# Performance work log

Hardware: AMD Instinct MI355X
Metric: run time of the kernel (lower is better)

## Reference

```python
import jax, jax.numpy as jnp
import numpy as np

EPS = 1e-10


def setup_inputs() -> dict:
    key = jax.random.key(0)
    ks = jax.random.split(key, 8)
    N, C, H, W = 32, 512, 14, 14
    D, HID = 2048, 256
    s1 = 1.0 / np.sqrt(C + D)
    s2 = 1.0 / np.sqrt(HID)
    return {
        "local_feature": jax.random.normal(ks[0], (N, C, H, W), jnp.float32),
        "global_feature": jax.random.normal(ks[1], (N, D, 1, 1), jnp.float32),
        "W1": jax.random.normal(ks[2], (C + D, HID), jnp.float32) * s1,
        "b1": jnp.zeros((HID,), jnp.float32),
        "W2": jax.random.normal(ks[3], (HID, HID), jnp.float32) * s2,
        "b2": jnp.zeros((HID,), jnp.float32),
        "W3": jax.random.normal(ks[4], (HID, 1), jnp.float32) * s2,
        "b3": jnp.zeros((1,), jnp.float32),
    }


def reference(local_feature, global_feature, W1, b1, W2, b2, W3, b3):
    # Vectorized form of DMIEstimator.calculate_mi (the per-sample Python loop
    # collapsed into one batched pass with a block-diagonal negative mask).
    N, C, H, W = local_feature.shape
    hw = H * W
    nhw = N * hw
    D = global_feature.shape[1]

    lf = jnp.transpose(local_feature, (0, 2, 3, 1)).reshape(nhw, C)   # [nhw, C]
    gf = global_feature[:, :, 0, 0]                                   # [N, D]

    # combined = cat([global, local], -1); split the first Linear accordingly
    # so the [N*nhw, C+D] concat tensor is never materialized.
    h_loc = lf @ W1[D:]                        # [nhw, HID]
    h_glb = gf @ W1[:D] + b1                   # [N, HID]
    h1 = jax.nn.relu(h_glb[:, None, :] + h_loc[None, :, :])  # [N, nhw, HID]
    h2 = jax.nn.relu(h1 @ W2 + b2)                            # [N, nhw, HID]
    scores = (h2 @ W3)[..., 0] + b3[0]                        # [N, nhw]

    mx = jnp.max(scores, axis=1, keepdims=True)               # [N, 1]
    ex = jnp.exp(scores - mx)

    # negatives for sample i exclude its own hw block [hw*i, hw*(i+1))
    own = (jnp.arange(nhw)[None, :] // hw) == jnp.arange(N)[:, None]  # [N, nhw]
    neg_mean = jnp.where(own, 0.0, ex).sum(axis=1) / (nhw - hw) + EPS  # [N]

    # positive (diagonal) block of scores: scores[i, hw*i : hw*(i+1)]
    pos = scores.reshape(N, N, hw)[jnp.arange(N), jnp.arange(N)]       # [N, hw]

    mi = pos - mx - jnp.log(neg_mean)[:, None]                         # [N, hw]
    return mi.reshape(N, H, W)
```

## Files before the change

kernel.cpp:

```cpp
#include <hip/hip_runtime.h>
#include <math.h>

#define NB   32
#define CC   512
#define DD   2048
#define HWP  196
#define NHW  6272
#define HID  256

typedef _Float16 h8 __attribute__((ext_vector_type(8)));
typedef _Float16 h4 __attribute__((ext_vector_type(4)));
typedef float    f4 __attribute__((ext_vector_type(4)));
typedef float    f16v __attribute__((ext_vector_type(16)));
union F4H8 { f4 f; h8 h; };

__global__ __launch_bounds__(256) void prep_kernel(const float* __restrict__ lf,
                                                   const float* __restrict__ gf,
                                                   const float* __restrict__ W1,
                                                   const float* __restrict__ W2,
                                                   float* __restrict__ hpart,
                                                   _Float16* __restrict__ W2G,
                                                   _Float16* __restrict__ W1F,
                                                   _Float16* __restrict__ lf16T) {
    int bid = blockIdx.x, tid = threadIdx.x;
    if (bid < 512) {
        int i = bid >> 4, ky = bid & 15, k = tid;
        const float* g = gf + (size_t)i * DD + ky * 128;
        const float* w = W1 + (size_t)(ky * 128) * HID + k;
        float a0 = 0.f, a1 = 0.f, a2 = 0.f, a3 = 0.f;
        #pragma unroll 8
        for (int r = 0; r < 128; r += 4) {
            a0 = fmaf(g[r + 0], w[(size_t)(r + 0) * HID], a0);
            a1 = fmaf(g[r + 1], w[(size_t)(r + 1) * HID], a1);
            a2 = fmaf(g[r + 2], w[(size_t)(r + 2) * HID], a2);
            a3 = fmaf(g[r + 3], w[(size_t)(r + 3) * HID], a3);
        }
        hpart[((size_t)i * 16 + ky) * HID + k] = (a0 + a1) + (a2 + a3);
    } else if (bid < 608) {
        int tg = (bid - 512) * 256 + tid;
        if (tg < 8192) {
            int t = tg, F = t >> 6, l = t & 63;
            int mt2 = F >> 4, ks = F & 15;
            int kb = ks * 16 + (l >> 5) * 8;
            int n  = mt2 * 32 + (l & 31);
            _Float16* o = W2G + (size_t)t * 8;
            #pragma unroll
            for (int j = 0; j < 8; j++) o[j] = (_Float16)W2[(size_t)(kb + j) * HID + n];
        } else {
            int t = tg - 8192, F = t >> 6, l = t & 63;
            int k2t = F >> 4, ks = F & 15;
            int kb = ks * 32 + (l >> 4) * 8;
            int n  = k2t * 16 + (l & 15);
            const float* W1c = W1 + (size_t)DD * HID;
            _Float16* o = W1F + (size_t)t * 8;
            #pragma unroll
            for (int j = 0; j < 8; j++) o[j] = (_Float16)W1c[(size_t)(kb + j) * HID + n];
        }
    } else {
        __shared__ _Float16 sT[64][HWP + 4];
        int b = bid - 608;
        int n = b >> 3, c0 = (b & 7) * 64;
        for (int task = tid; task < 64 * 49; task += 256) {
            int c = task / 49, f = task - c * 49;
            f4 v = *(const f4*)&lf[((size_t)n * CC + c0 + c) * HWP + f * 4];
            h4 o = { (_Float16)v.x, (_Float16)v.y, (_Float16)v.z, (_Float16)v.w };
            *(h4*)&sT[c][f * 4] = o;
        }
        __syncthreads();
        for (int task = tid; task < 8 * HWP; task += 256) {
            int ch = task / HWP, p = task - ch * HWP;
            h8 o;
            #pragma unroll
            for (int cc = 0; cc < 8; cc++) o[cc] = sT[ch * 8 + cc][p];
            *(h8*)&lf16T[((size_t)(n * HWP + p)) * CC + c0 + ch * 8] = o;
        }
    }
}

__global__ __launch_bounds__(256, 2) void hlocF_kernel(const _Float16* __restrict__ lf16T,
                                                       const _Float16* __restrict__ W1F,
                                                       const float* __restrict__ hpart,
                                                       const float* __restrict__ b1,
                                                       _Float16* __restrict__ g16,
                                                       _Float16* __restrict__ hL) {
    if (blockIdx.x == 196) {
        int kh = blockIdx.y;
        for (int x = threadIdx.x; x < 16 * HID; x += 256) {
            int i = kh * 16 + (x >> 8), k = x & 255;
            float s = b1[k];
            #pragma unroll
            for (int ky = 0; ky < 16; ky++) s += hpart[((size_t)i * 16 + ky) * HID + k];
            g16[(size_t)i * HID + k] = (_Float16)s;
        }
        return;
    }
    __shared__ _Float16 sLf[32][CC + 16];
    int tid = threadIdx.x;
    int w = tid >> 6, l = tid & 63, quad = l >> 4, ln = l & 15;
    int j0 = blockIdx.x * 32;
    int khalf = blockIdx.y;

    #pragma unroll
    for (int s = 0; s < 8; s++) {
        int y = s * 256 + tid;
        int row = y >> 6, col = (y & 63) * 8;
        h8 v = *(const h8*)&lf16T[(size_t)(j0 + row) * CC + col];
        *(h8*)&sLf[row][col] = v;
    }

    F4H8 Af[32];
    {
        const f4* src = (const f4*)W1F + l;
        #pragma unroll
        for (int mt = 0; mt < 2; mt++)
            #pragma unroll
            for (int ks = 0; ks < 16; ks++)
                Af[mt * 16 + ks].f = src[(size_t)((khalf * 8 + w * 2 + mt) * 16 + ks) * 64];
    }
    __syncthreads();

    f4 acc[4] = {};
    #pragma unroll
    for (int ks = 0; ks < 16; ks++) {
        h8 bF[2];
        #pragma unroll
        for (int nt = 0; nt < 2; nt++)
            bF[nt] = *(const h8*)&sLf[nt * 16 + ln][ks * 32 + quad * 8];
        #pragma unroll
        for (int mt = 0; mt < 2; mt++)
            #pragma unroll
            for (int nt = 0; nt < 2; nt++)
                acc[mt * 2 + nt] = __builtin_amdgcn_mfma_f32_16x16x32_f16(Af[mt * 16 + ks].h, bF[nt], acc[mt * 2 + nt], 0, 0, 0);
    }

    #pragma unroll
    for (int mt = 0; mt < 2; mt++)
        #pragma unroll
        for (int nt = 0; nt < 2; nt++) {
            int j  = j0 + nt * 16 + ln;
            int k2 = khalf * 128 + w * 32 + mt * 16 + quad * 4;
            h4 o = { (_Float16)acc[mt * 2 + nt][0], (_Float16)acc[mt * 2 + nt][1],
                     (_Float16)acc[mt * 2 + nt][2], (_Float16)acc[mt * 2 + nt][3] };
            *(h4*)&hL[(size_t)j * HID + k2] = o;
        }
}

__global__ __launch_bounds__(256, 2)
void score_kernel(const _Float16* __restrict__ hL,
                  const _Float16* __restrict__ g16,
                  const _Float16* __restrict__ W2G,
                  const float* __restrict__ b2,
                  const float* __restrict__ W3,
                  const float* __restrict__ b3,
                  float* __restrict__ scores) {
    __shared__ _Float16 sB[64 * HID];
    __shared__ float sRed[4][68];
    int tid = threadIdx.x, w = tid >> 6, l = tid & 63;
    int hi = l >> 5, ln32 = l & 31;
    int i0 = blockIdx.x * 2, jt = blockIdx.y;
    int j0 = jt * 64;

    F4H8 Af[2][16];
    {
        const f4* src = (const f4*)W2G + l;
        #pragma unroll
        for (int a = 0; a < 2; a++)
            #pragma unroll
            for (int ks = 0; ks < 16; ks++)
                Af[a][ks].f = src[(size_t)((w * 2 + a) * 16 + ks) * 64];
    }
    float bias3 = b3[0];

    int sj = tid >> 2, so = (tid & 3) * 8;
    const _Float16* hrow = hL + ((size_t)(j0 + sj)) * HID + so * 8;

    #pragma unroll 1
    for (int ii = 0; ii < 2; ii++) {
        int i = i0 + ii;
        const _Float16* grow = g16 + (size_t)i * HID + so * 8;
        h8 z = {};
        #pragma unroll
        for (int oi = 0; oi < 8; oi++) {
            int o = so + oi;
            h8 hv = *(const h8*)&hrow[oi * 8];
            h8 gq = *(const h8*)&grow[oi * 8];
            h8 h1 = __builtin_elementwise_max(hv + gq, z);
            int cell = ((sj >> 5) * 16 + (o >> 1)) * 512 + ((o & 1) * 32 + (sj & 31)) * 8;
            *(h8*)&sB[cell] = h1;
        }
        __syncthreads();

        #pragma unroll 1
        for (int ntg = 0; ntg < 2; ntg++) {
            f16v acc[2] = {};
            #pragma unroll
            for (int ks = 0; ks < 16; ks++) {
                h8 bz = *(const h8*)&sB[((ntg * 16 + ks) * 64 + l) * 8];
                acc[0] = __builtin_amdgcn_mfma_f32_32x32x16_f16(Af[0][ks].h, bz, acc[0], 0, 0, 0);
                acc[1] = __builtin_amdgcn_mfma_f32_32x32x16_f16(Af[1][ks].h, bz, acc[1], 0, 0, 0);
            }
            float s = 0.f;
            #pragma unroll
            for (int a = 0; a < 2; a++) {
                int kb = w * 64 + a * 32 + 4 * hi;
                #pragma unroll
                for (int q = 0; q < 4; q++) {
                    f4 b2v = *(const f4*)&b2[kb + q * 8];
                    f4 w3v = *(const f4*)&W3[kb + q * 8];
                    s += fmaxf(acc[a][q * 4 + 0] + b2v.x, 0.f) * w3v.x
                       + fmaxf(acc[a][q * 4 + 1] + b2v.y, 0.f) * w3v.y
                       + fmaxf(acc[a][q * 4 + 2] + b2v.z, 0.f) * w3v.z
                       + fmaxf(acc[a][q * 4 + 3] + b2v.w, 0.f) * w3v.w;
                }
            }
            s += __shfl_xor(s, 32, 64);
            if (hi == 0) sRed[w][ntg * 32 + ln32] = s;
        }
        __syncthreads();
        if (tid < 64) {
            scores[(size_t)i * NHW + j0 + tid] =
                sRed[0][tid] + sRed[1][tid] + sRed[2][tid] + sRed[3][tid] + bias3;
        }
    }
}

__global__ __launch_bounds__(1024) void reduce_kernel(const float* __restrict__ scores,
                                                      float* __restrict__ out) {
    int i = blockIdx.x, tid = threadIdx.x;
    const float* row = scores + (size_t)i * NHW;
    const f4* row4 = (const f4*)row;
    __shared__ float sM[16], sT[16], sO[16], sval[1];
    int q0 = i * 49, q1 = q0 + 49;
    float m = -1e30f, t = 0.f, o = 0.f;
    for (int q = tid; q < 1568; q += 1024) {
        f4 v = row4[q];
        float vm = fmaxf(fmaxf(v.x, v.y), fmaxf(v.z, v.w));
        float nm = fmaxf(m, vm);
        float sc = expf(m - nm);
        float e = expf(v.x - nm) + expf(v.y - nm) + expf(v.z - nm) + expf(v.w - nm);
        t = t * sc + e;
        o *= sc;
        if (q >= q0 && q < q1) o += e;
        m = nm;
    }
    #pragma unroll
    for (int off = 32; off > 0; off >>= 1) {
        float m2 = __shfl_xor(m, off, 64);
        float t2 = __shfl_xor(t, off, 64);
        float o2 = __shfl_xor(o, off, 64);
        float nm = fmaxf(m, m2);
        float sa = expf(m - nm), sb = expf(m2 - nm);
        t = t * sa + t2 * sb;
        o = o * sa + o2 * sb;
        m = nm;
    }
    if ((tid & 63) == 0) { sM[tid >> 6] = m; sT[tid >> 6] = t; sO[tid >> 6] = o; }
    __syncthreads();
    if (tid == 0) {
        float M = sM[0], T = sT[0], O = sO[0];
        for (int c = 1; c < 16; c++) {
            float nm = fmaxf(M, sM[c]);
            float sa = expf(M - nm), sb = expf(sM[c] - nm);
            T = T * sa + sT[c] * sb;
            O = O * sa + sO[c] * sb;
            M = nm;
        }
        float neg_mean = (T - O) / (float)(NHW - HWP) + 1e-10f;
        sval[0] = M + logf(neg_mean);
    }
    __syncthreads();
    float sub = sval[0];
    if (tid < HWP) out[(size_t)i * HWP + tid] = row[i * HWP + tid] - sub;
}

extern "C" void kernel_launch(void* const* d_in, const int* in_sizes, int n_in,
                              void* d_out, int out_size, void* d_ws, size_t ws_size,
                              hipStream_t stream) {
    const float* lf = (const float*)d_in[0];
    const float* gf = (const float*)d_in[1];
    const float* W1 = (const float*)d_in[2];
    const float* b1 = (const float*)d_in[3];
    const float* W2 = (const float*)d_in[4];
    const float* b2 = (const float*)d_in[5];
    const float* W3 = (const float*)d_in[6];
    const float* b3 = (const float*)d_in[7];
    float* out = (float*)d_out;

    char* ws = (char*)d_ws;
    _Float16* hL     = (_Float16*)ws;
    _Float16* g16    = (_Float16*)(ws + 3211264);
    _Float16* W2G    = (_Float16*)(ws + 3227648);
    _Float16* W1F    = (_Float16*)(ws + 3358720);
    _Float16* lf16T  = (_Float16*)(ws + 3620864);
    float*    scores = (float*)   (ws + 10043392);
    float*    hpart  = (float*)   (ws + 10846208);

    hipLaunchKernelGGL(prep_kernel, dim3(864), dim3(256), 0, stream,
                       lf, gf, W1, W2, hpart, W2G, W1F, lf16T);
    hipLaunchKernelGGL(hlocF_kernel, dim3(197, 2), dim3(256), 0, stream,
                       lf16T, W1F, hpart, b1, g16, hL);
    hipLaunchKernelGGL(score_kernel, dim3(16, 98), dim3(256), 0, stream,
                       hL, g16, W2G, b2, W3, b3, scores);
    hipLaunchKernelGGL(reduce_kernel, dim3(NB), dim3(1024), 0, stream, scores, out);
}
```

Baseline: 148.0 us.

## Double-buffer relu(h+g) LDS staging across the two samples per block

Splits the shared B tile into two buffers and builds the relu(hL + g) tiles for both samples of the block up front. The second sample's build is issued before the first sample's MFMA loop, so its global loads can overlap that compute, and one barrier per iteration is removed. The staging thread-to-element mapping also changes so each lane writes a contiguous 16-byte slot in LDS. In exchange LDS use per block roughly doubles, which may limit how many blocks fit on a CU alongside the two-per-CU launch bound.

```diff
diff --git a/kernel.cpp b/kernel.cpp
--- a/kernel.cpp
+++ b/kernel.cpp
@@ -153,7 +153,7 @@
                   const float* __restrict__ W3,
                   const float* __restrict__ b3,
                   float* __restrict__ scores) {
-    __shared__ _Float16 sB[64 * HID];
+    __shared__ _Float16 sB[2][64 * HID];
     __shared__ float sRed[4][68];
     int tid = threadIdx.x, w = tid >> 6, l = tid & 63;
     int hi = l >> 5, ln32 = l & 31;
@@ -170,32 +170,35 @@
                 Af[a][ks].f = src[(size_t)((w * 2 + a) * 16 + ks) * 64];
     }
     float bias3 = b3[0];
-
-    int sj = tid >> 2, so = (tid & 3) * 8;
-    const _Float16* hrow = hL + ((size_t)(j0 + sj)) * HID + so * 8;
+    h8 z = {};
+    int fb = (tid >> 6) * 8;
+
+    #define STAGE(BUF, I)                                                              \
+    {                                                                                  \
+        const _Float16* gB = g16 + (size_t)(I) * HID;                                  \
+        _Pragma("unroll")                                                              \
+        for (int r = 0; r < 8; r++) {                                                  \
+            int f = fb + r;                                                            \
+            int j = ((f >> 4) << 5) + (l & 31);                                        \
+            int o = ((f & 15) << 1) + hi;                                              \
+            h8 hv = *(const h8*)&hL[(size_t)(j0 + j) * HID + o * 8];                   \
+            h8 gq = *(const h8*)&gB[o * 8];                                            \
+            *(h8*)&sB[BUF][f * 512 + l * 8] = __builtin_elementwise_max(hv + gq, z);   \
+        }                                                                              \
+    }
+
+    STAGE(0, i0);
+    __syncthreads();
+    STAGE(1, i0 + 1);
 
     #pragma unroll 1
     for (int ii = 0; ii < 2; ii++) {
-        int i = i0 + ii;
-        const _Float16* grow = g16 + (size_t)i * HID + so * 8;
-        h8 z = {};
-        #pragma unroll
-        for (int oi = 0; oi < 8; oi++) {
-            int o = so + oi;
-            h8 hv = *(const h8*)&hrow[oi * 8];
-            h8 gq = *(const h8*)&grow[oi * 8];
-            h8 h1 = __builtin_elementwise_max(hv + gq, z);
-            int cell = ((sj >> 5) * 16 + (o >> 1)) * 512 + ((o & 1) * 32 + (sj & 31)) * 8;
-            *(h8*)&sB[cell] = h1;
-        }
-        __syncthreads();
-
         #pragma unroll 1
         for (int ntg = 0; ntg < 2; ntg++) {
             f16v acc[2] = {};
             #pragma unroll
             for (int ks = 0; ks < 16; ks++) {
-                h8 bz = *(const h8*)&sB[((ntg * 16 + ks) * 64 + l) * 8];
+                h8 bz = *(const h8*)&sB[ii][(ntg * 16 + ks) * 512 + l * 8];
                 acc[0] = __builtin_amdgcn_mfma_f32_32x32x16_f16(Af[0][ks].h, bz, acc[0], 0, 0, 0);
                 acc[1] = __builtin_amdgcn_mfma_f32_32x32x16_f16(Af[1][ks].h, bz, acc[1], 0, 0, 0);
             }
@@ -218,10 +221,12 @@
         }
         __syncthreads();
         if (tid < 64) {
-            scores[(size_t)i * NHW + j0 + tid] =
+            scores[(size_t)(i0 + ii) * NHW + j0 + tid] =
                 sRed[0][tid] + sRed[1][tid] + sRed[2][tid] + sRed[3][tid] + bias3;
         }
-    }
+        if (ii == 0) __syncthreads();
+    }
+    #undef STAGE
 }
 
 __global__ __launch_bounds__(1024) void reduce_kernel(const float* __restrict__ scores,
```

Measured after the change: 128.8 us. 1.15x faster.
